# Optimization experiments

Hardware: AMD Instinct MI355X
Metric: run time of the kernel (lower is better)

Reference implementation:

```python
import jax, jax.numpy as jnp
import numpy as np

B, H, S, DK, DV = 2, 48, 2048, 128, 128
EPS = 1e-6

def _l2norm(x):
    n = jnp.linalg.norm(x, axis=-1, keepdims=True)
    return x / jnp.maximum(n, EPS)

def setup_inputs() -> dict:
    root = jax.random.key(0)
    k0, k1, k2, k3, k4 = jax.random.split(root, 5)
    query = jax.random.normal(k0, (B, H, S, DK), jnp.float32)
    key = jax.random.normal(k1, (B, H, S, DK), jnp.float32)
    value = jax.random.normal(k2, (B, H, S, DV), jnp.float32)
    # g is a per-token log decay: negative, in (-0.5, 0)
    g = -0.5 * jax.random.uniform(k3, (B, H, S), jnp.float32)
    # beta is a sigmoid-like mixing gate in (0, 1)
    beta = jax.random.uniform(k4, (B, H, S), jnp.float32)
    return {"query": query, "key": key, "value": value, "g": g, "beta": beta}

def reference(query, key, value, g, beta):
    """Gated delta-rule linear-attention recurrence.

    state_t = state_{t-1} * exp(g_t)
    delta_t = (v_t - k_t^T state_t) * beta_t
    state_t = state_t + k_t delta_t^T
    out_t   = q_t^T state_t
    with q, k L2-normalized and q scaled by 1/sqrt(dk).
    Returns (output [B,H,S,DV], final_state [B,H,DK,DV]).
    """
    dk = query.shape[-1]
    scale = 1.0 / np.sqrt(dk).astype(np.float32)
    q = _l2norm(query) * scale
    k = _l2norm(key)
    # move seq axis to front for scan: (S, B, H, d)
    qs = jnp.moveaxis(q, 2, 0)
    ks = jnp.moveaxis(k, 2, 0)
    vs = jnp.moveaxis(value, 2, 0)
    gs = jnp.moveaxis(g, 2, 0)
    bs = jnp.moveaxis(beta, 2, 0)

    def step(state, xs):
        q_t, k_t, v_t, g_t, b_t = xs
        state = state * jnp.exp(g_t)[..., None, None]          # [B,H,DK,DV]
        kv_mem = jnp.einsum('bhk,bhkv->bhv', k_t, state)       # read
        delta = (v_t - kv_mem) * b_t[..., None]                # beta-scaled delta
        state = state + jnp.einsum('bhk,bhv->bhkv', k_t, delta)
        out = jnp.einsum('bhk,bhkv->bhv', q_t, state)
        return state, out

    init = jnp.zeros((query.shape[0], query.shape[1], dk, value.shape[-1]), query.dtype)
    final_state, outs = jax.lax.scan(step, init, (qs, ks, vs, gs, bs))
    output = jnp.moveaxis(outs, 0, 2)  # [B,H,S,DV]
    return output, final_state
```

## Files before the change

### kernel.cpp

```cpp
#include <hip/hip_runtime.h>

typedef __attribute__((ext_vector_type(8)))  short short8;
typedef __attribute__((ext_vector_type(4)))  float f32x4;
typedef __attribute__((ext_vector_type(16))) float f32x16;
typedef __attribute__((ext_vector_type(4)))  unsigned short ushort4v;

#define NH   96
#define SEQL 2048
#define DD   128
#define CC   64
#define NCH  32
#define SK   136
#define S64  72
#define SLOT 4608

__device__ __forceinline__ unsigned short f2bf(float f){
  union { float f; unsigned u; } v; v.f = f;
  unsigned r = v.u + 0x7FFFu + ((v.u >> 16) & 1u);
  return (unsigned short)(r >> 16);
}
__device__ __forceinline__ float bf2f(unsigned short u){
  union { unsigned u; float f; } v; v.u = ((unsigned)u) << 16; return v.f;
}
__device__ __forceinline__ short8 frg(const unsigned short* b, int stride, int row0, int kt, int lane){
  return *(const short8*)&b[(row0 + (lane & 31)) * stride + (kt << 4) + ((lane >> 5) << 3)];
}
__device__ __forceinline__ short8 ifrag(int n0, int kt, int lane){
  const int idx = n0 + (lane & 31) - (kt << 4) - ((lane >> 5) << 3);
  short8 v;
  #pragma unroll
  for (int e = 0; e < 8; ++e) v[e] = (short)((e == idx) ? 0x3F80 : 0);
  return v;
}
#define MM32(A,B,C) __builtin_amdgcn_mfma_f32_32x32x16_bf16(A,B,C,0,0,0)
__device__ __forceinline__ f32x16 z16(){
  return (f32x16){0.f,0.f,0.f,0.f,0.f,0.f,0.f,0.f,0.f,0.f,0.f,0.f,0.f,0.f,0.f,0.f};
}
template<int KTN>
__device__ __forceinline__ f32x16 gemm32(const unsigned short* A, int sa, int m0,
                                         const unsigned short* B, int sb, int n0,
                                         f32x16 acc, int lane){
  #pragma unroll
  for (int kt = 0; kt < KTN; ++kt)
    acc = MM32(frg(A, sa, m0, kt, lane), frg(B, sb, n0, kt, lane), acc);
  return acc;
}
__device__ __forceinline__ void stq(unsigned short* buf, int stride, int n0, int m0, int lane, f32x16 v){
  const int nn = n0 + (lane & 31), hh = (lane >> 5) << 2;
  #pragma unroll
  for (int q = 0; q < 4; ++q) {
    ushort4v pv;
    #pragma unroll
    for (int s = 0; s < 4; ++s) pv[s] = f2bf(v[4*q + s]);
    *(ushort4v*)&buf[nn * stride + m0 + 8*q + hh] = pv;
  }
}
__device__ __forceinline__ f32x16 ldq(const unsigned short* buf, int stride, int n0, int m0, int lane){
  f32x16 a;
  const int nn = n0 + (lane & 31), hh = (lane >> 5) << 2;
  #pragma unroll
  for (int q = 0; q < 4; ++q) {
    ushort4v pv = *(const ushort4v*)&buf[nn * stride + m0 + 8*q + hh];
    #pragma unroll
    for (int s = 0; s < 4; ++s) a[4*q + s] = bf2f(pv[s]);
  }
  return a;
}
__device__ __forceinline__ f32x16 pinit(const unsigned short* lo, const unsigned short* hi,
                                        int nt, int m0, int lane){
  const unsigned short* base = (nt ? hi : lo) + (lane & 31) * S64;
  const int hh = (lane >> 5) << 2;
  f32x16 p;
  #pragma unroll
  for (int q = 0; q < 4; ++q) {
    ushort4v t = *(const ushort4v*)&base[m0 + 8*q + hh];
    #pragma unroll
    for (int s = 0; s < 4; ++s) p[4*q + s] = bf2f(t[s]);
  }
  return p;
}
#define BAR() do { asm volatile("s_waitcnt lgkmcnt(0)" ::: "memory"); __builtin_amdgcn_s_barrier(); } while(0)

#define REC  36864
#define QOFF 0
#define WOFF 8192
#define UOFF 16384
#define KOFF 24576
#define MOFF 32768

#define AOF 0
#define BOF 9216
#define XS0 17920
#define XS1 22528
#define XS2 27136
#define XS3 31744
#define MRO 36352

__global__ __launch_bounds__(256, 2)
void gdn_prep(const float* __restrict__ Qg, const float* __restrict__ Kg,
              const float* __restrict__ Vg, const float* __restrict__ Gg,
              const float* __restrict__ Bg,
              unsigned short* __restrict__ wsp, float* __restrict__ wcs)
{
  __shared__ unsigned short a[40448];
  __shared__ float s_swv[64], s_swiv[64], s_sbe[64];

  const int tid = threadIdx.x, w = tid >> 6, lane = tid & 63;
  const int mt = w >> 1, nt = w & 1;
  const int hc = blockIdx.x, head = hc >> 5, c = hc & 31;
  const int t0 = c * CC;
  const size_t rb = (size_t)head * SEQL * DD + (size_t)t0 * DD;
  const float* kp = Kg + rb;
  const float* qp = Qg + rb;
  const float* vp = Vg + rb;
  const float* gp = Gg + (size_t)head * SEQL + t0;
  const float* bp = Bg + (size_t)head * SEQL + t0;
  unsigned short* rec = wsp + (size_t)hc * REC;

  const int lrow = tid >> 2, cb = (tid & 3) * 32;
  const int cq16 = (tid & 3) * 16;

  f32x4 kr[8], qr[8], vr[8];
  #pragma unroll
  for (int i = 0; i < 8; ++i) {
    kr[i] = *(const f32x4*)(kp + (size_t)lrow * DD + cb + 4*i);
    qr[i] = *(const f32x4*)(qp + (size_t)lrow * DD + cb + 4*i);
    vr[i] = *(const f32x4*)(vp + (size_t)lrow * DD + cb + 4*i);
  }
  float gl = gp[lane], bl = bp[lane];
  float sc = gl;
  #pragma unroll
  for (int d = 1; d < 64; d <<= 1) { float t = __shfl_up(sc, d); if (lane >= d) sc += t; }
  float wv = __expf(sc);
  if (w == 0) { s_swv[lane] = wv; s_swiv[lane] = __expf(-sc); s_sbe[lane] = bl; }
  float ssk = 0.f, ssq = 0.f;
  #pragma unroll
  for (int i = 0; i < 8; ++i) {
    ssk += kr[i][0]*kr[i][0] + kr[i][1]*kr[i][1] + kr[i][2]*kr[i][2] + kr[i][3]*kr[i][3];
    ssq += qr[i][0]*qr[i][0] + qr[i][1]*qr[i][1] + qr[i][2]*qr[i][2] + qr[i][3]*qr[i][3];
  }
  ssk += __shfl_xor(ssk, 1); ssk += __shfl_xor(ssk, 2);
  ssq += __shfl_xor(ssq, 1); ssq += __shfl_xor(ssq, 2);
  const float ik = 1.f / fmaxf(sqrtf(ssk), 1e-6f);
  const float wl = __shfl(wv, lrow);
  const float iq = 0.08838834764831845f / fmaxf(sqrtf(ssq), 1e-6f) * wl;
  #pragma unroll
  for (int i = 0; i < 8; ++i) {
    ushort4v pk, pq;
    #pragma unroll
    for (int r = 0; r < 4; ++r) { pk[r] = f2bf(kr[i][r]*ik); pq[r] = f2bf(qr[i][r]*iq); }
    *(ushort4v*)&a[AOF + lrow*SK + cb + 4*i] = pk;
    *(ushort4v*)&a[BOF + lrow*SK + cb + 4*i] = pq;
    *(ushort4v*)(rec + QOFF + lrow*DD + cb + 4*i) = pq;
  }
  BAR();

  {
    f32x16 ckk = gemm32<8>(a+AOF, SK, 32*mt, a+AOF, SK, 32*nt, z16(), lane);
    f32x16 ckq = gemm32<8>(a+AOF, SK, 32*mt, a+BOF, SK, 32*nt, z16(), lane);
    const int nn = 32*nt + (lane & 31), hh = (lane >> 5) << 2;
    const float ben = s_sbe[nn], wvn = s_swv[nn], sin = s_swiv[nn];
    #pragma unroll
    for (int q = 0; q < 4; ++q) {
      ushort4v xT, xR, mv;
      #pragma unroll
      for (int si = 0; si < 4; ++si) {
        const int r = 4*q + si, mm = 32*mt + 8*q + hh + si;
        const float svm = s_swv[mm], sim = s_swiv[mm], bem = s_sbe[mm];
        xT[si] = (mm > nn) ? f2bf(bem*svm*sin*ckk[r]) : 0;
        xR[si] = (nn > mm) ? f2bf(ben*wvn*sim*ckk[r]) : 0;
        mv[si] = (mm <= nn) ? f2bf(ckq[r]*sim) : 0;
      }
      const int off = nn*S64 + 32*mt + 8*q + hh;
      *(ushort4v*)&a[XS1 + off] = xT;
      *(ushort4v*)&a[XS0 + off] = xR;
      *(ushort4v*)(rec + MOFF + nn*64 + 32*mt + 8*q + hh) = mv;
    }
  }
  BAR();

  {
    f32x16 c1 = gemm32<4>(a+XS0, S64, 32*mt, a+XS1, S64, 32*nt, z16(), lane);
    f32x16 c2 = gemm32<4>(a+XS1, S64, 32*mt, a+XS0, S64, 32*nt, z16(), lane);
    stq(a+XS3, S64, 32*nt, 32*mt, lane, c1);
    stq(a+XS2, S64, 32*nt, 32*mt, lane, c2);
    unsigned short* p0 = a + ((lrow < 32) ? BOF : BOF+2304) + (lrow & 31)*S64;
    const unsigned short* x0 = a + XS0 + lrow*S64;
    #pragma unroll
    for (int jj = 0; jj < 2; ++jj) {
      short8 xv = *(const short8*)&x0[cq16 + 8*jj];
      short8 ov;
      #pragma unroll
      for (int e = 0; e < 8; ++e) {
        const int col = cq16 + 8*jj + e;
        ov[e] = (short)f2bf(((col == lrow) ? 1.f : 0.f) - bf2f((unsigned short)xv[e]));
      }
      *(short8*)&p0[cq16 + 8*jj] = ov;
    }
  }
  BAR();

  #pragma unroll
  for (int lev = 0; lev < 2; ++lev) {
    const int sr = (lev & 1) ? XS0 : XS2;
    const int st = (lev & 1) ? XS1 : XS3;
    const int dr = (lev & 1) ? XS2 : XS0;
    const int dt = (lev & 1) ? XS3 : XS1;
    const int pp = lev & 1;
    unsigned short* plo_s = a + (pp ? BOF+SLOT : BOF);
    unsigned short* phi_s = a + (pp ? MRO : BOF+2304);
    unsigned short* plo_d = a + (pp ? BOF : BOF+SLOT);
    unsigned short* phi_d = a + (pp ? BOF+2304 : MRO);
    f32x16 c1 = gemm32<4>(a+sr, S64, 32*mt, a+st, S64, 32*nt, z16(), lane);
    if (lev < 1) {
      f32x16 c2 = gemm32<4>(a+st, S64, 32*mt, a+sr, S64, 32*nt, z16(), lane);
      stq(a+dt, S64, 32*nt, 32*mt, lane, c1);
      stq(a+dr, S64, 32*nt, 32*mt, lane, c2);
    } else {
      stq(a+XS2, S64, 32*nt, 32*mt, lane, c1);
    }
    f32x16 p = pinit(plo_s, phi_s, nt, 32*mt, lane);
    p = gemm32<4>(a+st, S64, 32*mt, (nt ? phi_s : plo_s), S64, 0, p, lane);
    stq((nt ? phi_d : plo_d), S64, 0, 32*mt, lane, p);
    BAR();
  }

  {
    f32x16 p = pinit(a+BOF, a+BOF+2304, nt, 32*mt, lane);
    p = gemm32<4>(a+XS2, S64, 32*mt, (nt ? a+BOF+2304 : a+BOF), S64, 0, p, lane);
    stq((nt ? a+MRO : a+BOF+SLOT), S64, 0, 32*mt, lane, p);
    #pragma unroll
    for (int i = 0; i < 8; ++i)
      #pragma unroll
      for (int r = 0; r < 4; ++r)
        a[XS0 + (cb + 4*i + r)*S64 + lrow] = f2bf(vr[i][r]);
  }
  BAR();

  {
    unsigned short* trow  = a + ((lrow < 32) ? BOF+SLOT : MRO) + (lrow & 31)*S64;
    unsigned short* t3row = a + ((lrow < 32) ? BOF : BOF+2304) + (lrow & 31)*S64;
    #pragma unroll
    for (int jj = 0; jj < 2; ++jj) {
      short8 tv = *(const short8*)&trow[cq16 + 8*jj];
      short8 o2, o3;
      #pragma unroll
      for (int e = 0; e < 8; ++e) {
        const int j = cq16 + 8*jj + e;
        const float t = bf2f((unsigned short)tv[e]);
        o2[e] = (short)f2bf(-t * s_sbe[j] * s_swv[j]);
        o3[e] = (short)f2bf( t * s_sbe[j]);
      }
      *(short8*)&trow[cq16 + 8*jj]  = o2;
      *(short8*)&t3row[cq16 + 8*jj] = o3;
    }
    const float wcv = s_swv[63];
    #pragma unroll
    for (int j = 0; j < 2; ++j) {
      f32x16 ckt = z16();
      #pragma unroll
      for (int kk = 0; kk < 2; ++kk) {
        const int kt = 2*w + kk;
        ckt = MM32(frg(a+AOF, SK, 32*j, kt, lane), ifrag(32*w, kt, lane), ckt);
      }
      stq(a+XS2, S64, 32*w, 32*j, lane, ckt);
      const int nn = 32*w + (lane & 31), hh = (lane >> 5) << 2;
      #pragma unroll
      for (int q = 0; q < 4; ++q) {
        ushort4v o;
        #pragma unroll
        for (int si = 0; si < 4; ++si) {
          const int tok = 32*j + 8*q + hh + si;
          o[si] = f2bf(ckt[4*q+si] * wcv * s_swiv[tok]);
        }
        *(ushort4v*)(rec + KOFF + nn*64 + 32*j + 8*q + hh) = o;
      }
    }
  }
  BAR();

  {
    const int nn = lane & 31, hh = (lane >> 5) << 2;
    #pragma unroll
    for (int j = 0; j < 2; ++j) {
      f32x16 cw = gemm32<4>(a+XS2, S64, 32*w, (j ? a+MRO : a+BOF+SLOT), S64, 0, z16(), lane);
      #pragma unroll
      for (int q = 0; q < 4; ++q) {
        ushort4v pw;
        #pragma unroll
        for (int si = 0; si < 4; ++si) pw[si] = f2bf(cw[4*q+si]);
        *(ushort4v*)(rec + WOFF + (32*j + nn)*128 + 32*w + 8*q + hh) = pw;
      }
      f32x16 cu = gemm32<4>((j ? a+BOF+2304 : a+BOF), S64, 0, a+XS0, S64, 32*w, z16(), lane);
      #pragma unroll
      for (int q = 0; q < 4; ++q) {
        ushort4v pu;
        #pragma unroll
        for (int si = 0; si < 4; ++si) pu[si] = f2bf(cu[4*q+si]);
        *(ushort4v*)(rec + UOFF + (32*w + nn)*64 + 32*j + 8*q + hh) = pu;
      }
    }
    if (tid == 0) wcs[hc] = s_swv[63];
  }
}

#define SU   72
#define OW0  0
#define OW1  8704
#define OK0  17408
#define OK1  26624
#define OU0  35840
#define OU1  40448
#define OM0  45056
#define OM1  49664
#define OS0  54272
#define OS1  62976
#define ODT  71680

__global__ __launch_bounds__(512, 1)
void gdn_scan(const unsigned short* __restrict__ wsp, const float* __restrict__ wcs,
              float* __restrict__ Out, float* __restrict__ FS)
{
  __shared__ unsigned short a[76288];

  const int tid = threadIdx.x, w = tid >> 6, lane = tid & 63;
  const int head = blockIdx.x % NH, vh = blockIdx.x / NH;
  const unsigned short* recs = wsp + (size_t)head * NCH * REC;
  const float* wcsh = wcs + head * NCH;
  float* op = Out + (size_t)head * SEQL * DD + vh * 64;

  const int mtS = w >> 1, ntS = w & 1;
  const bool outw = (w < 4);

  f32x16 s = z16();

  const int wr = tid >> 3, wc16 = (tid & 7) * 16;
  const int kr = tid >> 2, kc16 = (tid & 3) * 16;
  const int ur = tid >> 3, uc8 = (tid & 7) * 8;

  short8 stW0, stW1, stK0, stK1, stU, stM, qb[8];
  float wcn = 0.f;

  auto issue = [&](int c){
    const unsigned short* rec = recs + (size_t)c * REC;
    stW0 = *(const short8*)(rec + WOFF + wr*128 + wc16);
    stW1 = *(const short8*)(rec + WOFF + wr*128 + wc16 + 8);
    stK0 = *(const short8*)(rec + KOFF + kr*64 + kc16);
    stK1 = *(const short8*)(rec + KOFF + kr*64 + kc16 + 8);
    stU  = *(const short8*)(rec + UOFF + (vh*64 + ur)*64 + uc8);
    stM  = *(const short8*)(rec + MOFF + ur*64 + uc8);
    if (outw) {
      #pragma unroll
      for (int kt = 0; kt < 8; ++kt)
        qb[kt] = *(const short8*)(rec + QOFF + (32*mtS + (lane & 31))*DD + kt*16 + ((lane >> 5) << 3));
    }
    wcn = wcsh[c];
  };
  auto dswrite = [&](int par){
    unsigned short* bw = a + (par ? OW1 : OW0);
    *(short8*)&bw[wr*SK + wc16]     = stW0;
    *(short8*)&bw[wr*SK + wc16 + 8] = stW1;
    unsigned short* bk = a + (par ? OK1 : OK0);
    *(short8*)&bk[kr*SU + kc16]     = stK0;
    *(short8*)&bk[kr*SU + kc16 + 8] = stK1;
    unsigned short* bu = a + (par ? OU1 : OU0);
    *(short8*)&bu[ur*SU + uc8] = stU;
    unsigned short* bm = a + (par ? OM1 : OM0);
    *(short8*)&bm[ur*SU + uc8] = stM;
  };

  issue(0);
  float wc_cur = wcn;
  dswrite(0);
  stq(a+OS0, SK, 32*ntS, 32*mtS, lane, s);
  BAR();

  for (int c = 0; c < NCH; ++c) {
    const int cur = c & 1;
    const unsigned short* W_ = a + (cur ? OW1 : OW0);
    const unsigned short* K_ = a + (cur ? OK1 : OK0);
    const unsigned short* U_ = a + (cur ? OU1 : OU0);
    const unsigned short* M_ = a + (cur ? OM1 : OM0);
    const unsigned short* S_ = a + (cur ? OS1 : OS0);
    unsigned short* Sn       = a + (cur ? OS0 : OS1);

    f32x16 oq = z16();
    if (outw) {
      #pragma unroll
      for (int kt = 0; kt < 8; ++kt)
        oq = MM32(qb[kt], frg(S_, SK, 32*ntS, kt, lane), oq);
    }
    if (c < NCH-1) issue(c+1);

    {
      f32x16 d0 = gemm32<8>(W_, SK, 0,  S_, SK, 32*ntS, z16(), lane);
      f32x16 d1 = gemm32<8>(W_, SK, 32, S_, SK, 32*ntS, z16(), lane);
      const int nn = 32*ntS + (lane & 31), hh = (lane >> 5) << 2;
      #pragma unroll
      for (int q = 0; q < 4; ++q) {
        ushort4v u0 = *(const ushort4v*)&U_[nn*SU + 0  + 8*q + hh];
        ushort4v u1 = *(const ushort4v*)&U_[nn*SU + 32 + 8*q + hh];
        ushort4v p0, p1;
        #pragma unroll
        for (int si = 0; si < 4; ++si) {
          p0[si] = f2bf(d0[4*q+si] + bf2f(u0[si]));
          p1[si] = f2bf(d1[4*q+si] + bf2f(u1[si]));
        }
        *(ushort4v*)&a[ODT + nn*SU + 0  + 8*q + hh] = p0;
        *(ushort4v*)&a[ODT + nn*SU + 32 + 8*q + hh] = p1;
      }
    }

    {
      f32x16 sa;
      #pragma unroll
      for (int r = 0; r < 16; ++r) sa[r] = s[r] * wc_cur;
      s = gemm32<4>(K_, SU, 32*mtS, a+ODT, SU, 32*ntS, sa, lane);
    }

    if (outw) {
      f32x16 o = gemm32<4>(M_, SU, 32*mtS, a+ODT, SU, 32*ntS, oq, lane);
      const int vv = 32*ntS + (lane & 31), hh = (lane >> 5) << 2;
      float* ob = op + (size_t)(c*CC + 32*mtS) * DD + vv;
      #pragma unroll
      for (int q = 0; q < 4; ++q)
        #pragma unroll
        for (int si = 0; si < 4; ++si)
          ob[(size_t)(si + 8*q + hh) * DD] = o[4*q + si];
    }

    stq(Sn, SK, 32*ntS, 32*mtS, lane, s);
    if (c < NCH-1) dswrite(cur ^ 1);
    wc_cur = wcn;
    BAR();
  }

  {
    float* fsp = FS + (size_t)head * DD * DD + vh * 64;
    const int nn = 32*ntS + (lane & 31), hh = (lane >> 5) << 2;
    #pragma unroll
    for (int q = 0; q < 4; ++q)
      #pragma unroll
      for (int si = 0; si < 4; ++si)
        fsp[(size_t)(32*mtS + si + 8*q + hh) * DD + nn] = s[4*q + si];
  }
}

__global__ __launch_bounds__(512, 1)
void gdn_chunk2(const float* __restrict__ Qg, const float* __restrict__ Kg,
                const float* __restrict__ Vg, const float* __restrict__ Gg,
                const float* __restrict__ Bg,
                float* __restrict__ Out, float* __restrict__ FS)
{
  __shared__ __align__(16) unsigned short sKc[64*SK];
  __shared__ __align__(16) unsigned short sQc[64*SK];
  __shared__ __align__(16) unsigned short sS0T[64*SK];
  __shared__ __align__(16) unsigned short sVc[64*S64];
  __shared__ __align__(16) unsigned short sVT[64*S64];
  __shared__ __align__(16) unsigned short sM[64*S64];
  __shared__ __align__(16) unsigned short sAr[8*SLOT];
  __shared__ float sbe2[2][64], swv2[2][64], swiv2[2][64];

  const int tid  = threadIdx.x;
  const int w    = tid >> 6;
  const int lane = tid & 63;
  const int half = w >> 2;
  const int j    = w & 3;
  const int mt   = j >> 1, nt = j & 1;
  const int mtS  = w >> 1, ntS = w & 1;
  const int mtK  = w >> 2, ntK = w & 3;
  const int head = blockIdx.x % NH;
  const int vh   = blockIdx.x / NH;

  const size_t rb = (size_t)head * SEQL * DD;
  const float* qp = Qg + rb;
  const float* kp = Kg + rb;
  const float* vp = Vg + rb + vh * 64;
  const float* gp = Gg + (size_t)head * SEQL;
  const float* bp = Bg + (size_t)head * SEQL;
  float* op  = Out + rb + vh * 64;
  float* fsp = FS + (size_t)head * DD * DD + vh * 64;

  const int lrow = tid >> 3;
  const int c16  = (tid & 7) * 16;
  const int c8   = (tid & 7) * 8;

  unsigned short* const sl0 = sAr + 0*SLOT;
  unsigned short* const sl1 = sAr + 1*SLOT;
  unsigned short* const sl2 = sAr + 2*SLOT;
  unsigned short* const sl3 = sAr + 3*SLOT;
  unsigned short* const sl4 = sAr + 4*SLOT;
  unsigned short* const sl5 = sAr + 5*SLOT;
  unsigned short* const sl6 = sAr + 6*SLOT;
  unsigned short* const sl7 = sAr + 7*SLOT;

  f32x16 s = z16(), oacc = z16();
  f32x4 kr[4], qr[4], vr[2]; float gr = 0.f, br = 0.f;

  auto prefetch = [&](int t0p){
    const float* kb = kp + (size_t)(t0p + lrow) * DD + c16;
    const float* qb = qp + (size_t)(t0p + lrow) * DD + c16;
    const float* vb = vp + (size_t)(t0p + lrow) * DD + c8;
    #pragma unroll
    for (int i = 0; i < 4; ++i) { kr[i] = *(const f32x4*)(kb + 4*i); qr[i] = *(const f32x4*)(qb + 4*i); }
    #pragma unroll
    for (int i = 0; i < 2; ++i) vr[i] = *(const f32x4*)(vb + 4*i);
    if (w == 7) { gr = gp[t0p + lane]; br = bp[t0p + lane]; }
  };
  auto scan_to = [&](int p){
    if (w == 7) {
      float sc = gr;
      #pragma unroll
      for (int d = 1; d < 64; d <<= 1) { float t = __shfl_up(sc, d); if (lane >= d) sc += t; }
      swv2[p][lane]  = __expf(sc);
      swiv2[p][lane] = __expf(-sc);
      sbe2[p][lane]  = br;
    }
  };

  prefetch(0);
  scan_to(0);
  BAR();

  for (int tc = 0; tc < NCH; ++tc) {
    const int t0 = tc * CC;
    const int cur = tc & 1, nxt = cur ^ 1;
    {
      float ssk = 0.f, ssq = 0.f;
      #pragma unroll
      for (int i = 0; i < 4; ++i) {
        ssk += kr[i][0]*kr[i][0] + kr[i][1]*kr[i][1] + kr[i][2]*kr[i][2] + kr[i][3]*kr[i][3];
        ssq += qr[i][0]*qr[i][0] + qr[i][1]*qr[i][1] + qr[i][2]*qr[i][2] + qr[i][3]*qr[i][3];
      }
      ssk += __shfl_xor(ssk, 1); ssk += __shfl_xor(ssk, 2); ssk += __shfl_xor(ssk, 4);
      ssq += __shfl_xor(ssq, 1); ssq += __shfl_xor(ssq, 2); ssq += __shfl_xor(ssq, 4);
      const float ik = 1.f / fmaxf(sqrtf(ssk), 1e-6f);
      const float iq = 0.08838834764831845f / fmaxf(sqrtf(ssq), 1e-6f) * swv2[cur][lrow];
      #pragma unroll
      for (int i = 0; i < 4; ++i) {
        ushort4v pk, pq;
        #pragma unroll
        for (int r = 0; r < 4; ++r) { pk[r] = f2bf(kr[i][r] * ik); pq[r] = f2bf(qr[i][r] * iq); }
        *(ushort4v*)&sKc[lrow*SK + c16 + 4*i] = pk;
        *(ushort4v*)&sQc[lrow*SK + c16 + 4*i] = pq;
      }
      #pragma unroll
      for (int i = 0; i < 2; ++i) {
        ushort4v pv;
        #pragma unroll
        for (int r = 0; r < 4; ++r) pv[r] = f2bf(vr[i][r]);
        *(ushort4v*)&sVc[lrow*S64 + c8 + 4*i] = pv;
      }
    }
    stq(sS0T, SK, 32*ntS, 32*mtS, lane, s);
    prefetch(tc < NCH-1 ? (tc+1)*CC : t0);
    BAR();

    if (half == 0) {
      f32x16 aa = gemm32<8>(sKc, SK, 32*mt, sKc, SK, 32*nt, z16(), lane);
      const int nn = 32*nt + (lane & 31), hh = (lane >> 5) << 2;
      #pragma unroll
      for (int q = 0; q < 4; ++q) {
        ushort4v pR, pL, pPT, pP;
        #pragma unroll
        for (int si = 0; si < 4; ++si) {
          const int r = 4*q + si, mm = 32*mt + 8*q + hh + si;
          const float S = aa[r];
          const float av  = (mm > nn) ? sbe2[cur][mm]*swv2[cur][mm]*swiv2[cur][nn]*S : 0.f;
          const float atr = (nn > mm) ? sbe2[cur][nn]*swv2[cur][nn]*swiv2[cur][mm]*S : 0.f;
          pR[si]  = f2bf(av);
          pL[si]  = f2bf(atr);
          pPT[si] = f2bf(((mm==nn)?1.f:0.f) - av);
          pP[si]  = f2bf(((mm==nn)?1.f:0.f) - atr);
        }
        const int off = nn*S64 + 32*mt + 8*q + hh;
        *(ushort4v*)&sl1[off] = pR;
        *(ushort4v*)&sl0[off] = pL;
        *(ushort4v*)&sl5[off] = pPT;
        *(ushort4v*)&sl4[off] = pP;
      }
    } else {
      f32x16 aa = gemm32<8>(sKc, SK, 32*mt, sQc, SK, 32*nt, z16(), lane);
      const int nn = 32*nt + (lane & 31), hh = (lane >> 5) << 2;
      #pragma unroll
      for (int q = 0; q < 4; ++q) {
        ushort4v pv;
        #pragma unroll
        for (int si = 0; si < 4; ++si) {
          const int r = 4*q + si, mm = 32*mt + 8*q + hh + si;
          pv[si] = f2bf((mm <= nn) ? aa[r]*swiv2[cur][mm] : 0.f);
        }
        *(ushort4v*)&sM[nn*S64 + 32*mt + 8*q + hh] = pv;
      }
    }
    BAR();

    if (half == 0) {
      f32x16 aa = gemm32<4>(sl0, S64, 32*mt, sl1, S64, 32*nt, z16(), lane);
      stq(sl3, S64, 32*nt, 32*mt, lane, aa);
      f32x16 bb = z16();
      #pragma unroll
      for (int kk = 0; kk < 2; ++kk) {
        const int kt = 2*nt + kk;
        bb = MM32(frg(sVc, S64, 32*mt, kt, lane), ifrag(32*nt, kt, lane), bb);
      }
      stq(sVT, S64, 32*nt, 32*mt, lane, bb);
    } else {
      f32x16 aa = gemm32<4>(sl1, S64, 32*mt, sl0, S64, 32*nt, z16(), lane);
      stq(sl2, S64, 32*nt, 32*mt, lane, aa);
      oacc = gemm32<8>(sQc, SK, 32*mt, sS0T, SK, 32*nt, z16(), lane);
    }
    BAR();

    {
      unsigned short* const inL[3]   = { sl2, sl0, sl2 };
      unsigned short* const inR[3]   = { sl3, sl1, sl3 };
      unsigned short* const outL[3]  = { sl0, sl2, sl0 };
      unsigned short* const outR[3]  = { sl1, sl3, sl1 };
      unsigned short* const inP[3]   = { sl4, sl7, sl5 };
      unsigned short* const inPT[3]  = { sl5, sl6, sl4 };
      unsigned short* const outP[3]  = { sl7, sl5, sl7 };
      unsigned short* const outPT[3] = { sl6, sl4, sl6 };
      #pragma unroll
      for (int lev = 0; lev < 3; ++lev) {
        if (half == 0) {
          f32x16 aa = gemm32<4>(inL[lev], S64, 32*mt, inR[lev], S64, 32*nt, z16(), lane);
          stq(outR[lev], S64, 32*nt, 32*mt, lane, aa);
          f32x16 p = ldq(inPT[lev], S64, 32*nt, 32*mt, lane);
          p = gemm32<4>(inP[lev], S64, 32*mt, inR[lev], S64, 32*nt, p, lane);
          stq(outPT[lev], S64, 32*nt, 32*mt, lane, p);
        } else {
          f32x16 aa = gemm32<4>(inR[lev], S64, 32*mt, inL[lev], S64, 32*nt, z16(), lane);
          stq(outL[lev], S64, 32*nt, 32*mt, lane, aa);
          f32x16 p = ldq(inP[lev], S64, 32*nt, 32*mt, lane);
          p = gemm32<4>(inR[lev], S64, 32*mt, inP[lev], S64, 32*nt, p, lane);
          stq(outP[lev], S64, 32*nt, 32*mt, lane, p);
        }
        BAR();
      }
    }

    if (half == 0) {
      f32x16 aa = gemm32<4>(sl0, S64, 32*mt, sl1, S64, 32*nt, z16(), lane);
      stq(sl2, S64, 32*nt, 32*mt, lane, aa);
    } else {
      f32x16 p = ldq(sl7, S64, 32*nt, 32*mt, lane);
      p = gemm32<4>(sl1, S64, 32*mt, sl7, S64, 32*nt, p, lane);
      stq(sl4, S64, 32*nt, 32*mt, lane, p);
    }
    BAR();

    if (half == 0) {
      f32x16 p = ldq(sl4, S64, 32*nt, 32*mt, lane);
      p = gemm32<4>(sl2, S64, 32*mt, sl4, S64, 32*nt, p, lane);
      const int nn = 32*nt + (lane & 31), hh = (lane >> 5) << 2;
      #pragma unroll
      for (int q = 0; q < 4; ++q) {
        ushort4v p2, p3;
        #pragma unroll
        for (int si = 0; si < 4; ++si) {
          const int r = 4*q + si, mm = 32*mt + 8*q + hh + si;
          const float t = p[r];
          p2[si] = f2bf(-t * sbe2[cur][mm] * swv2[cur][mm]);
          p3[si] = f2bf( t * sbe2[cur][mm]);
        }
        const int off = nn*S64 + 32*mt + 8*q + hh;
        *(ushort4v*)&sl1[off] = p2;
        *(ushort4v*)&sl5[off] = p3;
      }
    } else {
      f32x16 zz = gemm32<8>(sKc, SK, 32*mt, sS0T, SK, 32*nt, z16(), lane);
      stq(sl0, S64, 32*nt, 32*mt, lane, zz);
    }
    {
      f32x16 aa = z16();
      #pragma unroll
      for (int kk = 0; kk < 2; ++kk) {
        const int kt = 2*ntK + kk;
        aa = MM32(frg(sKc, SK, 32*mtK, kt, lane), ifrag(32*ntK, kt, lane), aa);
      }
      stq(sl6, S64, 32*ntK, 32*mtK, lane, aa);
    }
    BAR();

    if (half == 0) {
      f32x16 d = gemm32<4>(sl5, S64, 32*mt, sVT, S64, 32*nt, z16(), lane);
      d = gemm32<4>(sl1, S64, 32*mt, sl0, S64, 32*nt, d, lane);
      const int nn = 32*nt + (lane & 31), hh = (lane >> 5) << 2;
      const float w63 = swv2[cur][63];
      #pragma unroll
      for (int q = 0; q < 4; ++q) {
        ushort4v pt, ps;
        #pragma unroll
        for (int si = 0; si < 4; ++si) {
          const int r = 4*q + si, mm = 32*mt + 8*q + hh + si;
          pt[si] = f2bf(d[r]);
          ps[si] = f2bf(d[r] * w63 * swiv2[cur][mm]);
        }
        const int off = nn*S64 + 32*mt + 8*q + hh;
        *(ushort4v*)&sl3[off] = pt;
        *(ushort4v*)&sl2[off] = ps;
      }
    }
    scan_to(nxt);
    {
      const float w63 = swv2[cur][63];
      #pragma unroll
      for (int r = 0; r < 16; ++r) s[r] *= w63;
    }
    BAR();

    s = gemm32<4>(sl6, S64, 32*mtS, sl2, S64, 32*ntS, s, lane);
    if (half == 1) {
      f32x16 o = oacc;
      o = gemm32<4>(sM, S64, 32*mt, sl3, S64, 32*nt, o, lane);
      const int nn = 32*nt + (lane & 31), hh = (lane >> 5) << 2;
      #pragma unroll
      for (int q = 0; q < 4; ++q)
        #pragma unroll
        for (int si = 0; si < 4; ++si)
          op[(size_t)(t0 + 32*mt + 8*q + hh + si) * DD + nn] = o[4*q + si];
    }
    BAR();
  }

  {
    const int nn = 32*ntS + (lane & 31), hh = (lane >> 5) << 2;
    #pragma unroll
    for (int q = 0; q < 4; ++q)
      #pragma unroll
      for (int si = 0; si < 4; ++si)
        fsp[(size_t)(32*mtS + 8*q + hh + si) * DD + nn] = s[4*q + si];
  }
}

extern "C" void kernel_launch(void* const* d_in, const int* in_sizes, int n_in,
                              void* d_out, int out_size, void* d_ws, size_t ws_size,
                              hipStream_t stream) {
  const float* Q = (const float*)d_in[0];
  const float* K = (const float*)d_in[1];
  const float* V = (const float*)d_in[2];
  const float* G = (const float*)d_in[3];
  const float* B = (const float*)d_in[4];
  float* Out = (float*)d_out;
  float* FS  = Out + (size_t)NH * SEQL * DD;

  const size_t WS_NEED = (size_t)NH * NCH * REC * 2 + (size_t)NH * NCH * 4;
  if (ws_size >= WS_NEED) {
    unsigned short* wsp = (unsigned short*)d_ws;
    float* wcs = (float*)(wsp + (size_t)NH * NCH * REC);
    hipLaunchKernelGGL(gdn_prep, dim3(NH*NCH), dim3(256), 0, stream, Q, K, V, G, B, wsp, wcs);
    hipLaunchKernelGGL(gdn_scan, dim3(NH*2), dim3(512), 0, stream, wsp, wcs, Out, FS);
  } else {
    hipLaunchKernelGGL(gdn_chunk2, dim3(NH*2), dim3(512), 0, stream, Q, K, V, G, B, Out, FS);
  }
}
```

Before: 257.7 us.

## Widen prep kernel to 512 threads and split paired GEMMs across wave halves

The chunk-prep kernel now runs with 8 waves per block instead of 4. The paired GEMMs (kk vs kq, the two triangular inverse products, and the P updates) are divided between the first and second groups of four waves instead of being computed serially by the same waves. The doubling-level loop is unrolled into explicit stages so both groups stay busy between barriers. The V load is deferred to later in the kernel to reduce register pressure, and the launch bounds move to (512,4). The risk is extra barriers and register limits from the higher occupancy target. Prep is only part of total time, since the sequential scan kernel is unchanged.

```diff
diff --git a/kernel.cpp b/kernel.cpp
--- a/kernel.cpp
+++ b/kernel.cpp
@@ -96,7 +96,7 @@
 #define XS3 31744
 #define MRO 36352
 
-__global__ __launch_bounds__(256, 2)
+__global__ __launch_bounds__(512, 4)
 void gdn_prep(const float* __restrict__ Qg, const float* __restrict__ Kg,
               const float* __restrict__ Vg, const float* __restrict__ Gg,
               const float* __restrict__ Bg,
@@ -106,7 +106,7 @@
   __shared__ float s_swv[64], s_swiv[64], s_sbe[64];
 
   const int tid = threadIdx.x, w = tid >> 6, lane = tid & 63;
-  const int mt = w >> 1, nt = w & 1;
+  const int mt = (w & 3) >> 1, nt = w & 1;
   const int hc = blockIdx.x, head = hc >> 5, c = hc & 31;
   const int t0 = c * CC;
   const size_t rb = (size_t)head * SEQL * DD + (size_t)t0 * DD;
@@ -117,15 +117,15 @@
   const float* bp = Bg + (size_t)head * SEQL + t0;
   unsigned short* rec = wsp + (size_t)hc * REC;
 
-  const int lrow = tid >> 2, cb = (tid & 3) * 32;
-  const int cq16 = (tid & 3) * 16;
-
-  f32x4 kr[8], qr[8], vr[8];
-  #pragma unroll
-  for (int i = 0; i < 8; ++i) {
-    kr[i] = *(const f32x4*)(kp + (size_t)lrow * DD + cb + 4*i);
-    qr[i] = *(const f32x4*)(qp + (size_t)lrow * DD + cb + 4*i);
-    vr[i] = *(const f32x4*)(vp + (size_t)lrow * DD + cb + 4*i);
+  const int lrow = tid >> 3;
+  const int c16  = (tid & 7) * 16;
+  const int c8p  = (tid & 7) * 8;
+
+  f32x4 kr[4], qr[4];
+  #pragma unroll
+  for (int i = 0; i < 4; ++i) {
+    kr[i] = *(const f32x4*)(kp + (size_t)lrow * DD + c16 + 4*i);
+    qr[i] = *(const f32x4*)(qp + (size_t)lrow * DD + c16 + 4*i);
   }
   float gl = gp[lane], bl = bp[lane];
   float sc = gl;
@@ -135,170 +135,176 @@
   if (w == 0) { s_swv[lane] = wv; s_swiv[lane] = __expf(-sc); s_sbe[lane] = bl; }
   float ssk = 0.f, ssq = 0.f;
   #pragma unroll
-  for (int i = 0; i < 8; ++i) {
+  for (int i = 0; i < 4; ++i) {
     ssk += kr[i][0]*kr[i][0] + kr[i][1]*kr[i][1] + kr[i][2]*kr[i][2] + kr[i][3]*kr[i][3];
     ssq += qr[i][0]*qr[i][0] + qr[i][1]*qr[i][1] + qr[i][2]*qr[i][2] + qr[i][3]*qr[i][3];
   }
-  ssk += __shfl_xor(ssk, 1); ssk += __shfl_xor(ssk, 2);
-  ssq += __shfl_xor(ssq, 1); ssq += __shfl_xor(ssq, 2);
+  ssk += __shfl_xor(ssk, 1); ssk += __shfl_xor(ssk, 2); ssk += __shfl_xor(ssk, 4);
+  ssq += __shfl_xor(ssq, 1); ssq += __shfl_xor(ssq, 2); ssq += __shfl_xor(ssq, 4);
   const float ik = 1.f / fmaxf(sqrtf(ssk), 1e-6f);
   const float wl = __shfl(wv, lrow);
   const float iq = 0.08838834764831845f / fmaxf(sqrtf(ssq), 1e-6f) * wl;
   #pragma unroll
-  for (int i = 0; i < 8; ++i) {
+  for (int i = 0; i < 4; ++i) {
     ushort4v pk, pq;
     #pragma unroll
     for (int r = 0; r < 4; ++r) { pk[r] = f2bf(kr[i][r]*ik); pq[r] = f2bf(qr[i][r]*iq); }
-    *(ushort4v*)&a[AOF + lrow*SK + cb + 4*i] = pk;
-    *(ushort4v*)&a[BOF + lrow*SK + cb + 4*i] = pq;
-    *(ushort4v*)(rec + QOFF + lrow*DD + cb + 4*i) = pq;
-  }
-  BAR();
-
-  {
+    *(ushort4v*)&a[AOF + lrow*SK + c16 + 4*i] = pk;
+    *(ushort4v*)&a[BOF + lrow*SK + c16 + 4*i] = pq;
+    *(ushort4v*)(rec + QOFF + lrow*DD + c16 + 4*i) = pq;
+  }
+  BAR();
+
+  if (w < 4) {
     f32x16 ckk = gemm32<8>(a+AOF, SK, 32*mt, a+AOF, SK, 32*nt, z16(), lane);
-    f32x16 ckq = gemm32<8>(a+AOF, SK, 32*mt, a+BOF, SK, 32*nt, z16(), lane);
     const int nn = 32*nt + (lane & 31), hh = (lane >> 5) << 2;
     const float ben = s_sbe[nn], wvn = s_swv[nn], sin = s_swiv[nn];
     #pragma unroll
     for (int q = 0; q < 4; ++q) {
-      ushort4v xT, xR, mv;
+      ushort4v xT, xR;
       #pragma unroll
       for (int si = 0; si < 4; ++si) {
         const int r = 4*q + si, mm = 32*mt + 8*q + hh + si;
         const float svm = s_swv[mm], sim = s_swiv[mm], bem = s_sbe[mm];
         xT[si] = (mm > nn) ? f2bf(bem*svm*sin*ckk[r]) : 0;
         xR[si] = (nn > mm) ? f2bf(ben*wvn*sim*ckk[r]) : 0;
-        mv[si] = (mm <= nn) ? f2bf(ckq[r]*sim) : 0;
       }
       const int off = nn*S64 + 32*mt + 8*q + hh;
       *(ushort4v*)&a[XS1 + off] = xT;
       *(ushort4v*)&a[XS0 + off] = xR;
+    }
+  } else {
+    f32x16 ckq = gemm32<8>(a+AOF, SK, 32*mt, a+BOF, SK, 32*nt, z16(), lane);
+    const int nn = 32*nt + (lane & 31), hh = (lane >> 5) << 2;
+    #pragma unroll
+    for (int q = 0; q < 4; ++q) {
+      ushort4v mv;
+      #pragma unroll
+      for (int si = 0; si < 4; ++si) {
+        const int r = 4*q + si, mm = 32*mt + 8*q + hh + si;
+        mv[si] = (mm <= nn) ? f2bf(ckq[r]*s_swiv[mm]) : 0;
+      }
       *(ushort4v*)(rec + MOFF + nn*64 + 32*mt + 8*q + hh) = mv;
     }
   }
   BAR();
 
+  f32x4 vr[4];
+  #pragma unroll
+  for (int i = 0; i < 4; ++i)
+    vr[i] = *(const f32x4*)(vp + (size_t)lrow * DD + c16 + 4*i);
+  if (w < 4) {
+    f32x16 c1 = gemm32<4>(a+XS0, S64, 32*mt, a+XS1, S64, 32*nt, z16(), lane);
+    stq(a+XS3, S64, 32*nt, 32*mt, lane, c1);
+  } else {
+    f32x16 c2 = gemm32<4>(a+XS1, S64, 32*mt, a+XS0, S64, 32*nt, z16(), lane);
+    stq(a+XS2, S64, 32*nt, 32*mt, lane, c2);
+  }
   {
-    f32x16 c1 = gemm32<4>(a+XS0, S64, 32*mt, a+XS1, S64, 32*nt, z16(), lane);
-    f32x16 c2 = gemm32<4>(a+XS1, S64, 32*mt, a+XS0, S64, 32*nt, z16(), lane);
-    stq(a+XS3, S64, 32*nt, 32*mt, lane, c1);
-    stq(a+XS2, S64, 32*nt, 32*mt, lane, c2);
     unsigned short* p0 = a + ((lrow < 32) ? BOF : BOF+2304) + (lrow & 31)*S64;
     const unsigned short* x0 = a + XS0 + lrow*S64;
-    #pragma unroll
-    for (int jj = 0; jj < 2; ++jj) {
-      short8 xv = *(const short8*)&x0[cq16 + 8*jj];
-      short8 ov;
-      #pragma unroll
-      for (int e = 0; e < 8; ++e) {
-        const int col = cq16 + 8*jj + e;
-        ov[e] = (short)f2bf(((col == lrow) ? 1.f : 0.f) - bf2f((unsigned short)xv[e]));
-      }
-      *(short8*)&p0[cq16 + 8*jj] = ov;
-    }
-  }
-  BAR();
-
-  #pragma unroll
-  for (int lev = 0; lev < 2; ++lev) {
-    const int sr = (lev & 1) ? XS0 : XS2;
-    const int st = (lev & 1) ? XS1 : XS3;
-    const int dr = (lev & 1) ? XS2 : XS0;
-    const int dt = (lev & 1) ? XS3 : XS1;
-    const int pp = lev & 1;
-    unsigned short* plo_s = a + (pp ? BOF+SLOT : BOF);
-    unsigned short* phi_s = a + (pp ? MRO : BOF+2304);
-    unsigned short* plo_d = a + (pp ? BOF : BOF+SLOT);
-    unsigned short* phi_d = a + (pp ? BOF+2304 : MRO);
-    f32x16 c1 = gemm32<4>(a+sr, S64, 32*mt, a+st, S64, 32*nt, z16(), lane);
-    if (lev < 1) {
-      f32x16 c2 = gemm32<4>(a+st, S64, 32*mt, a+sr, S64, 32*nt, z16(), lane);
-      stq(a+dt, S64, 32*nt, 32*mt, lane, c1);
-      stq(a+dr, S64, 32*nt, 32*mt, lane, c2);
-    } else {
-      stq(a+XS2, S64, 32*nt, 32*mt, lane, c1);
-    }
-    f32x16 p = pinit(plo_s, phi_s, nt, 32*mt, lane);
-    p = gemm32<4>(a+st, S64, 32*mt, (nt ? phi_s : plo_s), S64, 0, p, lane);
-    stq((nt ? phi_d : plo_d), S64, 0, 32*mt, lane, p);
-    BAR();
-  }
-
-  {
+    short8 xv = *(const short8*)&x0[c8p];
+    short8 ov;
+    #pragma unroll
+    for (int e = 0; e < 8; ++e) {
+      const int col = c8p + e;
+      ov[e] = (short)f2bf(((col == lrow) ? 1.f : 0.f) - bf2f((unsigned short)xv[e]));
+    }
+    *(short8*)&p0[c8p] = ov;
+  }
+  BAR();
+
+  if (w < 4) {
+    f32x16 c1 = gemm32<4>(a+XS2, S64, 32*mt, a+XS3, S64, 32*nt, z16(), lane);
+    stq(a+XS1, S64, 32*nt, 32*mt, lane, c1);
+    f32x16 p = pinit(a+BOF, a+BOF+2304, nt, 32*mt, lane);
+    p = gemm32<4>(a+XS3, S64, 32*mt, (nt ? a+BOF+2304 : a+BOF), S64, 0, p, lane);
+    stq((nt ? a+MRO : a+BOF+SLOT), S64, 0, 32*mt, lane, p);
+  } else {
+    f32x16 c2 = gemm32<4>(a+XS3, S64, 32*mt, a+XS2, S64, 32*nt, z16(), lane);
+    stq(a+XS0, S64, 32*nt, 32*mt, lane, c2);
+  }
+  BAR();
+
+  if (w < 4) {
+    f32x16 c1 = gemm32<4>(a+XS0, S64, 32*mt, a+XS1, S64, 32*nt, z16(), lane);
+    stq(a+XS2, S64, 32*nt, 32*mt, lane, c1);
+  } else {
+    f32x16 p = pinit(a+BOF+SLOT, a+MRO, nt, 32*mt, lane);
+    p = gemm32<4>(a+XS1, S64, 32*mt, (nt ? a+MRO : a+BOF+SLOT), S64, 0, p, lane);
+    stq((nt ? a+BOF+2304 : a+BOF), S64, 0, 32*mt, lane, p);
+  }
+  BAR();
+
+  if (w < 4) {
     f32x16 p = pinit(a+BOF, a+BOF+2304, nt, 32*mt, lane);
     p = gemm32<4>(a+XS2, S64, 32*mt, (nt ? a+BOF+2304 : a+BOF), S64, 0, p, lane);
     stq((nt ? a+MRO : a+BOF+SLOT), S64, 0, 32*mt, lane, p);
-    #pragma unroll
-    for (int i = 0; i < 8; ++i)
-      #pragma unroll
-      for (int r = 0; r < 4; ++r)
-        a[XS0 + (cb + 4*i + r)*S64 + lrow] = f2bf(vr[i][r]);
-  }
+  }
+  #pragma unroll
+  for (int i = 0; i < 4; ++i)
+    #pragma unroll
+    for (int r = 0; r < 4; ++r)
+      a[XS0 + (c16 + 4*i + r)*S64 + lrow] = f2bf(vr[i][r]);
   BAR();
 
   {
     unsigned short* trow  = a + ((lrow < 32) ? BOF+SLOT : MRO) + (lrow & 31)*S64;
     unsigned short* t3row = a + ((lrow < 32) ? BOF : BOF+2304) + (lrow & 31)*S64;
-    #pragma unroll
-    for (int jj = 0; jj < 2; ++jj) {
-      short8 tv = *(const short8*)&trow[cq16 + 8*jj];
-      short8 o2, o3;
-      #pragma unroll
-      for (int e = 0; e < 8; ++e) {
-        const int j = cq16 + 8*jj + e;
-        const float t = bf2f((unsigned short)tv[e]);
-        o2[e] = (short)f2bf(-t * s_sbe[j] * s_swv[j]);
-        o3[e] = (short)f2bf( t * s_sbe[j]);
-      }
-      *(short8*)&trow[cq16 + 8*jj]  = o2;
-      *(short8*)&t3row[cq16 + 8*jj] = o3;
-    }
+    short8 tv = *(const short8*)&trow[c8p];
+    short8 o2, o3;
+    #pragma unroll
+    for (int e = 0; e < 8; ++e) {
+      const int j = c8p + e;
+      const float t = bf2f((unsigned short)tv[e]);
+      o2[e] = (short)f2bf(-t * s_sbe[j] * s_swv[j]);
+      o3[e] = (short)f2bf( t * s_sbe[j]);
+    }
+    *(short8*)&trow[c8p]  = o2;
+    *(short8*)&t3row[c8p] = o3;
+  }
+  {
+    const int j = w >> 2, d4 = w & 3;
     const float wcv = s_swv[63];
-    #pragma unroll
-    for (int j = 0; j < 2; ++j) {
-      f32x16 ckt = z16();
-      #pragma unroll
-      for (int kk = 0; kk < 2; ++kk) {
-        const int kt = 2*w + kk;
-        ckt = MM32(frg(a+AOF, SK, 32*j, kt, lane), ifrag(32*w, kt, lane), ckt);
-      }
-      stq(a+XS2, S64, 32*w, 32*j, lane, ckt);
-      const int nn = 32*w + (lane & 31), hh = (lane >> 5) << 2;
-      #pragma unroll
-      for (int q = 0; q < 4; ++q) {
-        ushort4v o;
-        #pragma unroll
-        for (int si = 0; si < 4; ++si) {
-          const int tok = 32*j + 8*q + hh + si;
-          o[si] = f2bf(ckt[4*q+si] * wcv * s_swiv[tok]);
-        }
-        *(ushort4v*)(rec + KOFF + nn*64 + 32*j + 8*q + hh) = o;
-      }
+    f32x16 ckt = z16();
+    #pragma unroll
+    for (int kk = 0; kk < 2; ++kk) {
+      const int kt = 2*d4 + kk;
+      ckt = MM32(frg(a+AOF, SK, 32*j, kt, lane), ifrag(32*d4, kt, lane), ckt);
+    }
+    stq(a+XS2, S64, 32*d4, 32*j, lane, ckt);
+    const int nn = 32*d4 + (lane & 31), hh = (lane >> 5) << 2;
+    #pragma unroll
+    for (int q = 0; q < 4; ++q) {
+      ushort4v o;
+      #pragma unroll
+      for (int si = 0; si < 4; ++si) {
+        const int tok = 32*j + 8*q + hh + si;
+        o[si] = f2bf(ckt[4*q+si] * wcv * s_swiv[tok]);
+      }
+      *(ushort4v*)(rec + KOFF + nn*64 + 32*j + 8*q + hh) = o;
     }
   }
   BAR();
 
   {
+    const int j = w >> 2, d4 = w & 3;
     const int nn = lane & 31, hh = (lane >> 5) << 2;
-    #pragma unroll
-    for (int j = 0; j < 2; ++j) {
-      f32x16 cw = gemm32<4>(a+XS2, S64, 32*w, (j ? a+MRO : a+BOF+SLOT), S64, 0, z16(), lane);
-      #pragma unroll
-      for (int q = 0; q < 4; ++q) {
-        ushort4v pw;
-        #pragma unroll
-        for (int si = 0; si < 4; ++si) pw[si] = f2bf(cw[4*q+si]);
-        *(ushort4v*)(rec + WOFF + (32*j + nn)*128 + 32*w + 8*q + hh) = pw;
-      }
-      f32x16 cu = gemm32<4>((j ? a+BOF+2304 : a+BOF), S64, 0, a+XS0, S64, 32*w, z16(), lane);
-      #pragma unroll
-      for (int q = 0; q < 4; ++q) {
-        ushort4v pu;
-        #pragma unroll
-        for (int si = 0; si < 4; ++si) pu[si] = f2bf(cu[4*q+si]);
-        *(ushort4v*)(rec + UOFF + (32*w + nn)*64 + 32*j + 8*q + hh) = pu;
-      }
+    f32x16 cw = gemm32<4>(a+XS2, S64, 32*d4, (j ? a+MRO : a+BOF+SLOT), S64, 0, z16(), lane);
+    #pragma unroll
+    for (int q = 0; q < 4; ++q) {
+      ushort4v pw;
+      #pragma unroll
+      for (int si = 0; si < 4; ++si) pw[si] = f2bf(cw[4*q+si]);
+      *(ushort4v*)(rec + WOFF + (32*j + nn)*128 + 32*d4 + 8*q + hh) = pw;
+    }
+    f32x16 cu = gemm32<4>((j ? a+BOF+2304 : a+BOF), S64, 0, a+XS0, S64, 32*d4, z16(), lane);
+    #pragma unroll
+    for (int q = 0; q < 4; ++q) {
+      ushort4v pu;
+      #pragma unroll
+      for (int si = 0; si < 4; ++si) pu[si] = f2bf(cu[4*q+si]);
+      *(ushort4v*)(rec + UOFF + (32*d4 + nn)*64 + 32*j + 8*q + hh) = pu;
     }
     if (tid == 0) wcs[hc] = s_swv[63];
   }
@@ -749,7 +755,7 @@
   if (ws_size >= WS_NEED) {
     unsigned short* wsp = (unsigned short*)d_ws;
     float* wcs = (float*)(wsp + (size_t)NH * NCH * REC);
-    hipLaunchKernelGGL(gdn_prep, dim3(NH*NCH), dim3(256), 0, stream, Q, K, V, G, B, wsp, wcs);
+    hipLaunchKernelGGL(gdn_prep, dim3(NH*NCH), dim3(512), 0, stream, Q, K, V, G, B, wsp, wcs);
     hipLaunchKernelGGL(gdn_scan, dim3(NH*2), dim3(512), 0, stream, wsp, wcs, Out, FS);
   } else {
     hipLaunchKernelGGL(gdn_chunk2, dim3(NH*2), dim3(512), 0, stream, Q, K, V, G, B, Out, FS);
```

Measured after the change: 235.0 us. -8.8%, faster.
